# Kernel tuning notes

Measured on AMD Instinct MI355X. Metric: run time of the kernel, lower is better.

Reference implementation:

```python
import jax, jax.numpy as jnp
import numpy as np

N = 100000      # nodes
E = 1600000     # edges (avg degree 16)
F = 128         # nfeats
H = 4           # nheads
D = 16          # nhid // nheads
ALPHA = 0.2     # LeakyReLU negative slope


def setup_inputs() -> dict:
    key = jax.random.key(0)
    k0, k1, k2, k3, k4 = jax.random.split(key, 5)
    h = jax.random.normal(k0, (N, F), dtype=jnp.float32)
    src = jax.random.randint(k1, (E,), 0, N)
    dst = jax.random.randint(k2, (E,), 0, N)
    # per-head Linear W (xavier_uniform gain=1.414 approx) and attention vector a
    limW = 1.414 * np.sqrt(6.0 / (F + D))
    W = jax.random.uniform(k3, (H, F, D), jnp.float32, -limW, limW)
    Wb = jnp.zeros((H, D), jnp.float32)
    lima = 1.414 * np.sqrt(6.0 / (2 * D + 1))
    a = jax.random.uniform(k4, (H, 2 * D), jnp.float32, -lima, lima)
    ab = jnp.zeros((H,), jnp.float32)
    return {"h": h, "W": W, "Wb": Wb, "a": a, "ab": ab, "src": src, "dst": dst}


def reference(h, W, Wb, a, ab, src, dst):
    # Per-head linear projection (dropout is identity in eval mode)
    Wh = jnp.einsum('nf,hfd->nhd', h, W) + Wb          # [N,H,D]
    Whs = Wh[src]                                       # [E,H,D] gather src
    Whd = Wh[dst]                                       # [E,H,D] gather dst
    # e = leakyrelu(a . [Wh_src || Wh_dst])
    e = (jnp.einsum('ehd,hd->eh', Whs, a[:, :D]) +
         jnp.einsum('ehd,hd->eh', Whd, a[:, D:]) + ab)  # [E,H]
    e = jnp.where(e > 0, e, ALPHA * e)
    # segment softmax over incoming edges per dst node
    m = jax.ops.segment_max(e, dst, num_segments=N)     # [N,H]
    m = jnp.where(jnp.isfinite(m), m, 0.0)
    p = jnp.exp(e - m[dst])                             # [E,H]
    denom = jax.ops.segment_sum(p, dst, num_segments=N) # [N,H]
    num = jax.ops.segment_sum(p[:, :, None] * Whs, dst, num_segments=N)  # [N,H,D]
    h_prime = num / jnp.maximum(denom, 1e-9)[:, :, None]
    # concat heads -> [N, H*D]; rows of nodes with no in-edges are zero
    return h_prime.reshape(N, H * D)
```

## Files before the change

kernel.cpp:

```cpp
#include <hip/hip_runtime.h>
#include <hip/hip_bf16.h>
#include <math.h>

#define N_NODES 100000
#define N_EDGES 1600000
#define NF 128
#define NH 4
#define ND 16
#define GAT_ALPHA 0.2f

#define BSHIFT 8
#define NBK 391
#define CAPB 5120
#define CAPQ 1280
#define EPB 8192
#define EBLK 196
#define PBLK 391
#define NTILES ((N_NODES + 63) / 64)

typedef __attribute__((ext_vector_type(8))) __bf16 bf16x8;
typedef __attribute__((ext_vector_type(4))) float f32x4;

#define PADK 136

__global__ __launch_bounds__(256) void k_prep(
    const float* __restrict__ W, const float* __restrict__ a,
    int* __restrict__ gcur, __hip_bfloat16* __restrict__ Btg)
{
    const int hh = blockIdx.x;
    const int t = threadIdx.x;

    if (hh == 0)
        for (int i = t; i < 512; i += 256) gcur[i] = 0;

    for (int idx = t; idx < 2048; idx += 256) {
        int d = idx & 15, f = idx >> 4;
        Btg[(hh * 16 + d) * 128 + f] =
            __float2bfloat16(W[hh * (NF * ND) + f * ND + d]);
    }
    for (int idx = t; idx < 256; idx += 256) {
        int f = idx & 127, which = idx >> 7;
        float s = 0.f;
        #pragma unroll
        for (int d = 0; d < 16; d++)
            s = fmaf(W[hh * (NF * ND) + f * ND + d], a[hh * 32 + which * 16 + d], s);
        Btg[(64 + which * 8 + hh) * 128 + f] = __float2bfloat16(s);
    }
    for (int idx = t; idx < 256; idx += 256) {
        int f = idx & 127, which = idx >> 7;
        Btg[(68 + which * 8 + hh) * 128 + f] = __float2bfloat16(0.f);
    }
}

__global__ __launch_bounds__(256) void k_fused(
    const float* __restrict__ h, const __hip_bfloat16* __restrict__ Btg,
    const float* __restrict__ Wb, const float* __restrict__ a,
    const float* __restrict__ ab, const int* __restrict__ src,
    const int* __restrict__ dst, int* __restrict__ gcur,
    uint* __restrict__ sb, __hip_bfloat16* __restrict__ Whb,
    float* __restrict__ es, float* __restrict__ ed)
{
    __shared__ __align__(16) char smem[80 * PADK * 2];

    const int tid = threadIdx.x;

    if (blockIdx.x < EBLK) {
        int* hist = (int*)smem;
        int* cur  = hist + NBK;
        const int base = blockIdx.x * EPB;
        const int lim = min(EPB, N_EDGES - base);

        for (int i = tid; i < NBK; i += 256) hist[i] = 0;
        __syncthreads();
        for (int i = tid; i < lim; i += 256)
            atomicAdd(&hist[dst[base + i] >> BSHIFT], 1);
        __syncthreads();
        for (int i = tid; i < NBK; i += 256) {
            int v = hist[i];
            cur[i] = v ? atomicAdd(&gcur[i], v) : 0;
        }
        __syncthreads();
        for (int i = tid; i < lim; i += 256) {
            int d = dst[base + i];
            int bk = d >> BSHIFT;
            int pos = atomicAdd(&cur[bk], 1);
            if (pos < CAPB)
                sb[bk * CAPB + pos] = (uint)(src[base + i] | ((d & 255) << 17));
        }
        return;
    }

    __hip_bfloat16* Bt = (__hip_bfloat16*)smem;
    const int pb = blockIdx.x - EBLK;
    const int wv = tid >> 6;
    const int l = tid & 63;
    const int m = l & 15;
    const int quad = l >> 4;

    for (int c = tid; c < 80 * 128 / 8; c += 256) {
        int row = c >> 4, col = (c & 15) * 8;
        *(float4*)&Bt[row * PADK + col] = ((const float4*)Btg)[c];
    }

    float wb4[4];
    #pragma unroll
    for (int t = 0; t < 4; t++) wb4[t] = Wb[t * 16 + m];
    float eb = 0.f;
    if (m < 4) {
        #pragma unroll
        for (int d = 0; d < 16; d++) eb = fmaf(Wb[m * 16 + d], a[m * 32 + d], eb);
    } else if (m >= 8 && m < 12) {
        int hh = m - 8;
        #pragma unroll
        for (int d = 0; d < 16; d++)
            eb = fmaf(Wb[hh * 16 + d], a[hh * 32 + 16 + d], eb);
        eb += ab[hh];
    }
    __syncthreads();

    for (int tile = pb; tile < NTILES; tile += PBLK) {
        const int node = tile * 64 + wv * 16 + m;
        const bool ok = node < N_NODES;
        const float4* hrow = (const float4*)(h + (size_t)(ok ? node : 0) * NF);

        f32x4 acc[5];
        #pragma unroll
        for (int t = 0; t < 5; t++) acc[t] = (f32x4){0.f, 0.f, 0.f, 0.f};

        #pragma unroll
        for (int kk = 0; kk < 4; kk++) {
            bf16x8 af;
            if (ok) {
                float4 v0 = hrow[kk * 8 + quad * 2];
                float4 v1 = hrow[kk * 8 + quad * 2 + 1];
                af[0] = (__bf16)v0.x; af[1] = (__bf16)v0.y;
                af[2] = (__bf16)v0.z; af[3] = (__bf16)v0.w;
                af[4] = (__bf16)v1.x; af[5] = (__bf16)v1.y;
                af[6] = (__bf16)v1.z; af[7] = (__bf16)v1.w;
            } else {
                #pragma unroll
                for (int j = 0; j < 8; j++) af[j] = (__bf16)0.f;
            }
            #pragma unroll
            for (int t = 0; t < 5; t++) {
                bf16x8 bf = *(const bf16x8*)&Bt[(t * 16 + m) * PADK + kk * 32 + quad * 8];
                acc[t] = __builtin_amdgcn_mfma_f32_16x16x32_bf16(af, bf, acc[t], 0, 0, 0);
            }
        }

        const int nodeb = tile * 64 + wv * 16 + quad * 4;
        #pragma unroll
        for (int r = 0; r < 4; r++) {
            int n = nodeb + r;
            if (n < N_NODES) {
                #pragma unroll
                for (int t = 0; t < 4; t++)
                    Whb[n * 64 + t * 16 + m] = __float2bfloat16(acc[t][r] + wb4[t]);
                float ev = acc[4][r] + eb;
                if (m < 4) es[n * 4 + m] = ev;
                else if (m >= 8 && m < 12) ed[n * 4 + (m - 8)] = ev;
            }
        }
    }
}

__global__ __launch_bounds__(256) void k_bucket(
    const uint* __restrict__ sb, const int* __restrict__ gcur,
    const __hip_bfloat16* __restrict__ Whb, const float* __restrict__ es,
    const float* __restrict__ ed, float* __restrict__ out)
{
    __shared__ int ssl[CAPQ];
    __shared__ int ncnt[64];
    __shared__ int noff[64];
    __shared__ int ncur[64];
    __shared__ float pu_all[4][256];

    const int b  = blockIdx.x >> 2;
    const int qt = blockIdx.x & 3;
    const int t  = threadIdx.x;
    const int l  = t & 63;
    const int wid = t >> 6;

    const int ebase = b * CAPB;
    const int ecnt = min(gcur[b], CAPB);
    const int dlo = qt << 6;

    if (t < 64) ncnt[t] = 0;
    __syncthreads();

    for (int i = t; i < ecnt; i += 256) {
        int dn = (int)(sb[ebase + i] >> 17) - dlo;
        if ((unsigned)dn < 64u) atomicAdd(&ncnt[dn], 1);
    }
    __syncthreads();

    if (t < 64) {
        int v = ncnt[t];
        int x = v;
        #pragma unroll
        for (int o = 1; o < 64; o <<= 1) {
            int y = __shfl_up(x, o);
            if (l >= o) x += y;
        }
        noff[t] = x - v;
        ncur[t] = x - v;
    }
    __syncthreads();

    for (int i = t; i < ecnt; i += 256) {
        uint v = sb[ebase + i];
        int dn = (int)(v >> 17) - dlo;
        if ((unsigned)dn < 64u) {
            int pos = atomicAdd(&ncur[dn], 1);
            if (pos < CAPQ) ssl[pos] = (int)(v & 0x1FFFFu);
        }
    }
    __syncthreads();

    const int r = l & 15;
    const int q = l >> 4;
    const int hh = r >> 2;
    const float4* es4 = (const float4*)es;
    const uint2* Wu2 = (const uint2*)Whb;
    float* pu = &pu_all[wid][0];
    const float* pu_q = pu + q * 4 + hh;

    for (int k = 0; k < 16; k++) {
        const int ln = wid * 16 + k;
        const int node = b * 256 + dlo + ln;
        if (node >= N_NODES) break;

        int start = noff[ln];
        int deg = ncnt[ln];
        if (start >= CAPQ) deg = 0;
        else deg = min(deg, CAPQ - start);

        const float4 edv = ((const float4*)ed)[node];

        float acc0 = 0.f, acc1 = 0.f, acc2 = 0.f, acc3 = 0.f, den = 0.f;

        for (int bst = 0; bst < deg; bst += 64) {
            int nchunk = min(64, deg - bst);

            float4 p4 = make_float4(0.f, 0.f, 0.f, 0.f);
            if (l < nchunk) {
                int sl = ssl[start + bst + l];
                float4 esv = es4[sl];
                float x;
                x = esv.x + edv.x; p4.x = __expf(fmaxf(x, GAT_ALPHA * x));
                x = esv.y + edv.y; p4.y = __expf(fmaxf(x, GAT_ALPHA * x));
                x = esv.z + edv.z; p4.z = __expf(fmaxf(x, GAT_ALPHA * x));
                x = esv.w + edv.w; p4.w = __expf(fmaxf(x, GAT_ALPHA * x));
            }
            ((float4*)pu)[l] = p4;

            const int last = start + deg - 1;
            #pragma unroll 4
            for (int jj = 0; jj < nchunk; jj += 4) {
                int ee = min(start + bst + jj + q, last);
                int s = ssl[ee];
                float p = pu_q[jj * 4];
                uint2 v = Wu2[s * 16 + r];
                acc0 = fmaf(p, __uint_as_float(v.x << 16), acc0);
                acc1 = fmaf(p, __uint_as_float(v.x & 0xffff0000u), acc1);
                acc2 = fmaf(p, __uint_as_float(v.y << 16), acc2);
                acc3 = fmaf(p, __uint_as_float(v.y & 0xffff0000u), acc3);
                den += p;
            }
        }

        acc0 += __shfl_xor(acc0, 16); acc1 += __shfl_xor(acc1, 16);
        acc2 += __shfl_xor(acc2, 16); acc3 += __shfl_xor(acc3, 16);
        den  += __shfl_xor(den, 16);
        acc0 += __shfl_xor(acc0, 32); acc1 += __shfl_xor(acc1, 32);
        acc2 += __shfl_xor(acc2, 32); acc3 += __shfl_xor(acc3, 32);
        den  += __shfl_xor(den, 32);

        if (q == 0) {
            float rr = 1.0f / fmaxf(den, 1e-9f);
            ((float4*)out)[node * 16 + r] =
                make_float4(acc0 * rr, acc1 * rr, acc2 * rr, acc3 * rr);
        }
    }
}

extern "C" void kernel_launch(void* const* d_in, const int* in_sizes, int n_in,
                              void* d_out, int out_size, void* d_ws, size_t ws_size,
                              hipStream_t stream)
{
    const float* h  = (const float*)d_in[0];
    const float* W  = (const float*)d_in[1];
    const float* Wb = (const float*)d_in[2];
    const float* a  = (const float*)d_in[3];
    const float* ab = (const float*)d_in[4];
    const int* src  = (const int*)d_in[5];
    const int* dst  = (const int*)d_in[6];
    float* out = (float*)d_out;

    char* w = (char*)d_ws;
    __hip_bfloat16* Whb = (__hip_bfloat16*)w; w += (size_t)N_NODES * 64 * 2;
    float* es      = (float*)w;  w += (size_t)N_NODES * 4 * 4;
    float* ed      = (float*)w;  w += (size_t)N_NODES * 4 * 4;
    uint* sb       = (uint*)w;   w += (size_t)NBK * CAPB * 4;
    int* gcur      = (int*)w;    w += 512 * 4;
    __hip_bfloat16* Btg = (__hip_bfloat16*)w; w += 80 * 128 * 2;

    k_prep<<<4, 256, 0, stream>>>(W, a, gcur, Btg);
    k_fused<<<EBLK + PBLK, 256, 0, stream>>>(h, Btg, Wb, a, ab, src, dst,
                                             gcur, sb, Whb, es, ed);
    k_bucket<<<NBK * 4, 256, 0, stream>>>(sb, gcur, Whb, es, ed, out);
}
```

Before: 192.9 us.

## Give each projection tile its own block and widen gather to 16-byte loads

The projection part now launches one block per 64-node tile instead of a grid-stride loop, and issues the h row loads before the shared-memory weight staging so the global load latency overlaps that copy. The aggregation loop now has each lane gather 8 bf16 values (uint4) per source row instead of 4, covering 8 edges per wave step instead of 4. The shuffle reduction grows to three rounds over 9 values. This trades more blocks, each redoing the weight staging, and higher per-lane register use for fewer, wider memory transactions.

```diff
diff --git a/kernel.cpp b/kernel.cpp
--- a/kernel.cpp
+++ b/kernel.cpp
@@ -15,7 +15,7 @@
 #define CAPQ 1280
 #define EPB 8192
 #define EBLK 196
-#define PBLK 391
+#define PBLK 1563
 #define NTILES ((N_NODES + 63) / 64)
 
 typedef __attribute__((ext_vector_type(8))) __bf16 bf16x8;
@@ -91,12 +91,22 @@
     }
 
     __hip_bfloat16* Bt = (__hip_bfloat16*)smem;
-    const int pb = blockIdx.x - EBLK;
+    const int tile = blockIdx.x - EBLK;
     const int wv = tid >> 6;
     const int l = tid & 63;
     const int m = l & 15;
     const int quad = l >> 4;
 
+    const int node = tile * 64 + wv * 16 + m;
+    const bool ok = node < N_NODES;
+    const float4* hrow = (const float4*)(h + (size_t)(ok ? node : 0) * NF);
+    float4 va[8];
+    #pragma unroll
+    for (int kk = 0; kk < 4; kk++) {
+        va[kk * 2]     = hrow[kk * 8 + quad * 2];
+        va[kk * 2 + 1] = hrow[kk * 8 + quad * 2 + 1];
+    }
+
     for (int c = tid; c < 80 * 128 / 8; c += 256) {
         int row = c >> 4, col = (c & 15) * 8;
         *(float4*)&Bt[row * PADK + col] = ((const float4*)Btg)[c];
@@ -118,48 +128,41 @@
     }
     __syncthreads();
 
-    for (int tile = pb; tile < NTILES; tile += PBLK) {
-        const int node = tile * 64 + wv * 16 + m;
-        const bool ok = node < N_NODES;
-        const float4* hrow = (const float4*)(h + (size_t)(ok ? node : 0) * NF);
-
-        f32x4 acc[5];
-        #pragma unroll
-        for (int t = 0; t < 5; t++) acc[t] = (f32x4){0.f, 0.f, 0.f, 0.f};
-
-        #pragma unroll
-        for (int kk = 0; kk < 4; kk++) {
-            bf16x8 af;
-            if (ok) {
-                float4 v0 = hrow[kk * 8 + quad * 2];
-                float4 v1 = hrow[kk * 8 + quad * 2 + 1];
-                af[0] = (__bf16)v0.x; af[1] = (__bf16)v0.y;
-                af[2] = (__bf16)v0.z; af[3] = (__bf16)v0.w;
-                af[4] = (__bf16)v1.x; af[5] = (__bf16)v1.y;
-                af[6] = (__bf16)v1.z; af[7] = (__bf16)v1.w;
-            } else {
-                #pragma unroll
-                for (int j = 0; j < 8; j++) af[j] = (__bf16)0.f;
-            }
+    f32x4 acc[5];
+    #pragma unroll
+    for (int t = 0; t < 5; t++) acc[t] = (f32x4){0.f, 0.f, 0.f, 0.f};
+
+    #pragma unroll
+    for (int kk = 0; kk < 4; kk++) {
+        bf16x8 af;
+        if (ok) {
+            float4 v0 = va[kk * 2], v1 = va[kk * 2 + 1];
+            af[0] = (__bf16)v0.x; af[1] = (__bf16)v0.y;
+            af[2] = (__bf16)v0.z; af[3] = (__bf16)v0.w;
+            af[4] = (__bf16)v1.x; af[5] = (__bf16)v1.y;
+            af[6] = (__bf16)v1.z; af[7] = (__bf16)v1.w;
+        } else {
             #pragma unroll
-            for (int t = 0; t < 5; t++) {
-                bf16x8 bf = *(const bf16x8*)&Bt[(t * 16 + m) * PADK + kk * 32 + quad * 8];
-                acc[t] = __builtin_amdgcn_mfma_f32_16x16x32_bf16(af, bf, acc[t], 0, 0, 0);
-            }
-        }
-
-        const int nodeb = tile * 64 + wv * 16 + quad * 4;
-        #pragma unroll
-        for (int r = 0; r < 4; r++) {
-            int n = nodeb + r;
-            if (n < N_NODES) {
-                #pragma unroll
-                for (int t = 0; t < 4; t++)
-                    Whb[n * 64 + t * 16 + m] = __float2bfloat16(acc[t][r] + wb4[t]);
-                float ev = acc[4][r] + eb;
-                if (m < 4) es[n * 4 + m] = ev;
-                else if (m >= 8 && m < 12) ed[n * 4 + (m - 8)] = ev;
-            }
+            for (int j = 0; j < 8; j++) af[j] = (__bf16)0.f;
+        }
+        #pragma unroll
+        for (int t = 0; t < 5; t++) {
+            bf16x8 bf = *(const bf16x8*)&Bt[(t * 16 + m) * PADK + kk * 32 + quad * 8];
+            acc[t] = __builtin_amdgcn_mfma_f32_16x16x32_bf16(af, bf, acc[t], 0, 0, 0);
+        }
+    }
+
+    const int nodeb = tile * 64 + wv * 16 + quad * 4;
+    #pragma unroll
+    for (int r = 0; r < 4; r++) {
+        int n = nodeb + r;
+        if (n < N_NODES) {
+            #pragma unroll
+            for (int t = 0; t < 4; t++)
+                Whb[n * 64 + t * 16 + m] = __float2bfloat16(acc[t][r] + wb4[t]);
+            float ev = acc[4][r] + eb;
+            if (m < 4) es[n * 4 + m] = ev;
+            else if (m >= 8 && m < 12) ed[n * 4 + (m - 8)] = ev;
         }
     }
 }
@@ -217,13 +220,13 @@
     }
     __syncthreads();
 
-    const int r = l & 15;
-    const int q = l >> 4;
-    const int hh = r >> 2;
+    const int r8 = l & 7;
+    const int q8 = l >> 3;
+    const int hh8 = r8 >> 1;
     const float4* es4 = (const float4*)es;
-    const uint2* Wu2 = (const uint2*)Whb;
+    const uint4* Wu4 = (const uint4*)Whb;
     float* pu = &pu_all[wid][0];
-    const float* pu_q = pu + q * 4 + hh;
+    const float* pu_q8 = pu + q8 * 4 + hh8;
 
     for (int k = 0; k < 16; k++) {
         const int ln = wid * 16 + k;
@@ -237,7 +240,8 @@
 
         const float4 edv = ((const float4*)ed)[node];
 
-        float acc0 = 0.f, acc1 = 0.f, acc2 = 0.f, acc3 = 0.f, den = 0.f;
+        float ac0 = 0.f, ac1 = 0.f, ac2 = 0.f, ac3 = 0.f;
+        float ac4 = 0.f, ac5 = 0.f, ac6 = 0.f, ac7 = 0.f, den = 0.f;
 
         for (int bst = 0; bst < deg; bst += 64) {
             int nchunk = min(64, deg - bst);
@@ -256,30 +260,38 @@
 
             const int last = start + deg - 1;
             #pragma unroll 4
-            for (int jj = 0; jj < nchunk; jj += 4) {
-                int ee = min(start + bst + jj + q, last);
+            for (int jj = 0; jj < nchunk; jj += 8) {
+                int ee = min(start + bst + jj + q8, last);
                 int s = ssl[ee];
-                float p = pu_q[jj * 4];
-                uint2 v = Wu2[s * 16 + r];
-                acc0 = fmaf(p, __uint_as_float(v.x << 16), acc0);
-                acc1 = fmaf(p, __uint_as_float(v.x & 0xffff0000u), acc1);
-                acc2 = fmaf(p, __uint_as_float(v.y << 16), acc2);
-                acc3 = fmaf(p, __uint_as_float(v.y & 0xffff0000u), acc3);
+                float p = pu_q8[jj * 4];
+                uint4 v = Wu4[s * 8 + r8];
+                ac0 = fmaf(p, __uint_as_float(v.x << 16), ac0);
+                ac1 = fmaf(p, __uint_as_float(v.x & 0xffff0000u), ac1);
+                ac2 = fmaf(p, __uint_as_float(v.y << 16), ac2);
+                ac3 = fmaf(p, __uint_as_float(v.y & 0xffff0000u), ac3);
+                ac4 = fmaf(p, __uint_as_float(v.z << 16), ac4);
+                ac5 = fmaf(p, __uint_as_float(v.z & 0xffff0000u), ac5);
+                ac6 = fmaf(p, __uint_as_float(v.w << 16), ac6);
+                ac7 = fmaf(p, __uint_as_float(v.w & 0xffff0000u), ac7);
                 den += p;
             }
         }
 
-        acc0 += __shfl_xor(acc0, 16); acc1 += __shfl_xor(acc1, 16);
-        acc2 += __shfl_xor(acc2, 16); acc3 += __shfl_xor(acc3, 16);
-        den  += __shfl_xor(den, 16);
-        acc0 += __shfl_xor(acc0, 32); acc1 += __shfl_xor(acc1, 32);
-        acc2 += __shfl_xor(acc2, 32); acc3 += __shfl_xor(acc3, 32);
-        den  += __shfl_xor(den, 32);
-
-        if (q == 0) {
+        #pragma unroll
+        for (int o = 8; o < 64; o <<= 1) {
+            ac0 += __shfl_xor(ac0, o); ac1 += __shfl_xor(ac1, o);
+            ac2 += __shfl_xor(ac2, o); ac3 += __shfl_xor(ac3, o);
+            ac4 += __shfl_xor(ac4, o); ac5 += __shfl_xor(ac5, o);
+            ac6 += __shfl_xor(ac6, o); ac7 += __shfl_xor(ac7, o);
+            den += __shfl_xor(den, o);
+        }
+
+        if (q8 == 0) {
             float rr = 1.0f / fmaxf(den, 1e-9f);
-            ((float4*)out)[node * 16 + r] =
-                make_float4(acc0 * rr, acc1 * rr, acc2 * rr, acc3 * rr);
+            ((float4*)out)[node * 16 + r8 * 2] =
+                make_float4(ac0 * rr, ac1 * rr, ac2 * rr, ac3 * rr);
+            ((float4*)out)[node * 16 + r8 * 2 + 1] =
+                make_float4(ac4 * rr, ac5 * rr, ac6 * rr, ac7 * rr);
         }
     }
 }
```

Result: slower. 208.3 us (+8.0%).

## Process four destination nodes per wave with one quarter-wave per node

Applied to the files above, without the earlier changes.

The aggregation loop now gives each 16-lane quarter of a wave its own destination node, so a wave handles four nodes at once. Before, the whole wave worked on one node and needed cross-quarter shuffle reductions. The attention weights for all edges of the four nodes are computed together in one pass into a larger LDS buffer, which keeps more lanes busy than the old per-node 64-edge chunks. Destination scores are also preloaded into LDS once per block. The cost is serial per-lane loops whose length follows the largest degree in each group of four, and edges beyond 256 per group are silently dropped.

```diff
diff --git a/kernel.cpp b/kernel.cpp
--- a/kernel.cpp
+++ b/kernel.cpp
@@ -173,7 +173,8 @@
     __shared__ int ncnt[64];
     __shared__ int noff[64];
     __shared__ int ncur[64];
-    __shared__ float pu_all[4][256];
+    __shared__ float edl[64 * 4];
+    __shared__ float pu_all[4][256 * 4];
 
     const int b  = blockIdx.x >> 2;
     const int qt = blockIdx.x & 3;
@@ -185,7 +186,12 @@
     const int ecnt = min(gcur[b], CAPB);
     const int dlo = qt << 6;
 
-    if (t < 64) ncnt[t] = 0;
+    if (t < 64) {
+        ncnt[t] = 0;
+        int node = b * 256 + dlo + t;
+        ((float4*)edl)[t] = (node < N_NODES) ? ((const float4*)ed)[node]
+                                             : make_float4(0.f, 0.f, 0.f, 0.f);
+    }
     __syncthreads();
 
     for (int i = t; i < ecnt; i += 256) {
@@ -223,63 +229,63 @@
     const float4* es4 = (const float4*)es;
     const uint2* Wu2 = (const uint2*)Whb;
     float* pu = &pu_all[wid][0];
-    const float* pu_q = pu + q * 4 + hh;
-
-    for (int k = 0; k < 16; k++) {
-        const int ln = wid * 16 + k;
+
+    for (int kp = 0; kp < 4; kp++) {
+        const int base = wid * 16 + kp * 4;
+
+        int estart = min(noff[base], CAPQ);
+        int eend = min(noff[base + 3] + ncnt[base + 3], CAPQ);
+        int ecount = eend - estart;
+        if (ecount < 0) ecount = 0;
+        if (ecount > 256) ecount = 256;
+
+        const int off1 = noff[base + 1], off2 = noff[base + 2], off3 = noff[base + 3];
+
+        for (int e = l; e < ecount; e += 64) {
+            int gi = estart + e;
+            int sl = ssl[gi];
+            int nid = (gi >= off1) + (gi >= off2) + (gi >= off3);
+            const float4 edv = *(const float4*)&edl[(base + nid) * 4];
+            float4 esv = es4[sl];
+            float4 p4;
+            float x;
+            x = esv.x + edv.x; p4.x = __expf(fmaxf(x, GAT_ALPHA * x));
+            x = esv.y + edv.y; p4.y = __expf(fmaxf(x, GAT_ALPHA * x));
+            x = esv.z + edv.z; p4.z = __expf(fmaxf(x, GAT_ALPHA * x));
+            x = esv.w + edv.w; p4.w = __expf(fmaxf(x, GAT_ALPHA * x));
+            *(float4*)&pu[e * 4] = p4;
+        }
+
+        const int ln = base + q;
+        const int sbase = noff[ln];
+        int myoff = sbase - estart;
+        int deg = ncnt[ln];
+        if (sbase >= CAPQ) deg = 0;
+        else deg = min(deg, CAPQ - sbase);
+        {
+            int pucap = ecount - myoff;
+            if (pucap < 0) pucap = 0;
+            deg = min(deg, pucap);
+        }
+
+        float a0 = 0.f, a1 = 0.f, a2 = 0.f, a3 = 0.f, den = 0.f;
+        #pragma unroll 4
+        for (int j = 0; j < deg; j++) {
+            int s = ssl[sbase + j];
+            float p = pu[(myoff + j) * 4 + hh];
+            uint2 v = Wu2[s * 16 + r];
+            a0 = fmaf(p, __uint_as_float(v.x << 16), a0);
+            a1 = fmaf(p, __uint_as_float(v.x & 0xffff0000u), a1);
+            a2 = fmaf(p, __uint_as_float(v.y << 16), a2);
+            a3 = fmaf(p, __uint_as_float(v.y & 0xffff0000u), a3);
+            den += p;
+        }
+
         const int node = b * 256 + dlo + ln;
-        if (node >= N_NODES) break;
-
-        int start = noff[ln];
-        int deg = ncnt[ln];
-        if (start >= CAPQ) deg = 0;
-        else deg = min(deg, CAPQ - start);
-
-        const float4 edv = ((const float4*)ed)[node];
-
-        float acc0 = 0.f, acc1 = 0.f, acc2 = 0.f, acc3 = 0.f, den = 0.f;
-
-        for (int bst = 0; bst < deg; bst += 64) {
-            int nchunk = min(64, deg - bst);
-
-            float4 p4 = make_float4(0.f, 0.f, 0.f, 0.f);
-            if (l < nchunk) {
-                int sl = ssl[start + bst + l];
-                float4 esv = es4[sl];
-                float x;
-                x = esv.x + edv.x; p4.x = __expf(fmaxf(x, GAT_ALPHA * x));
-                x = esv.y + edv.y; p4.y = __expf(fmaxf(x, GAT_ALPHA * x));
-                x = esv.z + edv.z; p4.z = __expf(fmaxf(x, GAT_ALPHA * x));
-                x = esv.w + edv.w; p4.w = __expf(fmaxf(x, GAT_ALPHA * x));
-            }
-            ((float4*)pu)[l] = p4;
-
-            const int last = start + deg - 1;
-            #pragma unroll 4
-            for (int jj = 0; jj < nchunk; jj += 4) {
-                int ee = min(start + bst + jj + q, last);
-                int s = ssl[ee];
-                float p = pu_q[jj * 4];
-                uint2 v = Wu2[s * 16 + r];
-                acc0 = fmaf(p, __uint_as_float(v.x << 16), acc0);
-                acc1 = fmaf(p, __uint_as_float(v.x & 0xffff0000u), acc1);
-                acc2 = fmaf(p, __uint_as_float(v.y << 16), acc2);
-                acc3 = fmaf(p, __uint_as_float(v.y & 0xffff0000u), acc3);
-                den += p;
-            }
-        }
-
-        acc0 += __shfl_xor(acc0, 16); acc1 += __shfl_xor(acc1, 16);
-        acc2 += __shfl_xor(acc2, 16); acc3 += __shfl_xor(acc3, 16);
-        den  += __shfl_xor(den, 16);
-        acc0 += __shfl_xor(acc0, 32); acc1 += __shfl_xor(acc1, 32);
-        acc2 += __shfl_xor(acc2, 32); acc3 += __shfl_xor(acc3, 32);
-        den  += __shfl_xor(den, 32);
-
-        if (q == 0) {
+        if (node < N_NODES) {
             float rr = 1.0f / fmaxf(den, 1e-9f);
             ((float4*)out)[node * 16 + r] =
-                make_float4(acc0 * rr, acc1 * rr, acc2 * rr, acc3 * rr);
+                make_float4(a0 * rr, a1 * rr, a2 * rr, a3 * rr);
         }
     }
 }
```

Result: slower. 212.3 us (+10.0%).

## Fuse three kernels into one cooperative launch with grid-wide syncs

Applied to the files above, without the earlier changes.

Merges the prep, bucketing/projection, and per-bucket aggregation kernels into one cooperative kernel separated by grid.sync barriers, with a fallback to the original three launches. The aim is to remove two kernel launch gaps and the associated tail drain. In exchange, all 1564 blocks must be co-resident, so launch bounds force higher occupancy, which may cap registers. Grid barriers and idle blocks during the smaller phases add their own cost.

```diff
diff --git a/kernel.cpp b/kernel.cpp
--- a/kernel.cpp
+++ b/kernel.cpp
@@ -1,6 +1,9 @@
 #include <hip/hip_runtime.h>
 #include <hip/hip_bf16.h>
+#include <hip/hip_cooperative_groups.h>
 #include <math.h>
+
+namespace cg = cooperative_groups;
 
 #define N_NODES 100000
 #define N_EDGES 1600000
@@ -17,11 +20,270 @@
 #define EBLK 196
 #define PBLK 391
 #define NTILES ((N_NODES + 63) / 64)
+#define GRID_ALL (NBK * 4)
 
 typedef __attribute__((ext_vector_type(8))) __bf16 bf16x8;
 typedef __attribute__((ext_vector_type(4))) float f32x4;
 
 #define PADK 136
+
+__global__ __launch_bounds__(256, 8) void k_all(
+    const float* __restrict__ h, const float* __restrict__ W,
+    const float* __restrict__ Wb, const float* __restrict__ a,
+    const float* __restrict__ ab, const int* __restrict__ src,
+    const int* __restrict__ dst, int* __restrict__ gcur,
+    uint* __restrict__ sb, __hip_bfloat16* __restrict__ Whb,
+    float* __restrict__ es, float* __restrict__ ed,
+    __hip_bfloat16* __restrict__ Btg, float* __restrict__ out)
+{
+    cg::grid_group grid = cg::this_grid();
+    __shared__ __align__(16) char smem[80 * PADK * 2];
+
+    const int tid = threadIdx.x;
+    const int bid = blockIdx.x;
+    const int l = tid & 63;
+    const int wid = tid >> 6;
+
+    if (bid < 4) {
+        const int hh = bid;
+        if (hh == 0)
+            for (int i = tid; i < 512; i += 256) gcur[i] = 0;
+        for (int idx = tid; idx < 2048; idx += 256) {
+            int d = idx & 15, f = idx >> 4;
+            Btg[(hh * 16 + d) * 128 + f] =
+                __float2bfloat16(W[hh * (NF * ND) + f * ND + d]);
+        }
+        for (int idx = tid; idx < 256; idx += 256) {
+            int f = idx & 127, which = idx >> 7;
+            float s = 0.f;
+            #pragma unroll
+            for (int d = 0; d < 16; d++)
+                s = fmaf(W[hh * (NF * ND) + f * ND + d],
+                         a[hh * 32 + which * 16 + d], s);
+            Btg[(64 + which * 8 + hh) * 128 + f] = __float2bfloat16(s);
+        }
+        for (int idx = tid; idx < 256; idx += 256) {
+            int f = idx & 127, which = idx >> 7;
+            Btg[(68 + which * 8 + hh) * 128 + f] = __float2bfloat16(0.f);
+        }
+    }
+    grid.sync();
+
+    if (bid < EBLK) {
+        int* hist = (int*)smem;
+        int* cur  = hist + NBK;
+        const int base = bid * EPB;
+        const int lim = min(EPB, N_EDGES - base);
+
+        for (int i = tid; i < NBK; i += 256) hist[i] = 0;
+        __syncthreads();
+        for (int i = tid; i < lim; i += 256)
+            atomicAdd(&hist[dst[base + i] >> BSHIFT], 1);
+        __syncthreads();
+        for (int i = tid; i < NBK; i += 256) {
+            int v = hist[i];
+            cur[i] = v ? atomicAdd(&gcur[i], v) : 0;
+        }
+        __syncthreads();
+        for (int i = tid; i < lim; i += 256) {
+            int d = dst[base + i];
+            int bk = d >> BSHIFT;
+            int pos = atomicAdd(&cur[bk], 1);
+            if (pos < CAPB)
+                sb[bk * CAPB + pos] = (uint)(src[base + i] | ((d & 255) << 17));
+        }
+    } else if (bid < EBLK + PBLK) {
+        __hip_bfloat16* Bt = (__hip_bfloat16*)smem;
+        const int pb = bid - EBLK;
+        const int m = l & 15;
+        const int quad = l >> 4;
+
+        for (int c = tid; c < 80 * 128 / 8; c += 256) {
+            int row = c >> 4, col = (c & 15) * 8;
+            *(float4*)&Bt[row * PADK + col] = ((const float4*)Btg)[c];
+        }
+
+        float wb4[4];
+        #pragma unroll
+        for (int t = 0; t < 4; t++) wb4[t] = Wb[t * 16 + m];
+        float eb = 0.f;
+        if (m < 4) {
+            #pragma unroll
+            for (int d = 0; d < 16; d++)
+                eb = fmaf(Wb[m * 16 + d], a[m * 32 + d], eb);
+        } else if (m >= 8 && m < 12) {
+            int hh = m - 8;
+            #pragma unroll
+            for (int d = 0; d < 16; d++)
+                eb = fmaf(Wb[hh * 16 + d], a[hh * 32 + 16 + d], eb);
+            eb += ab[hh];
+        }
+        __syncthreads();
+
+        for (int tile = pb; tile < NTILES; tile += PBLK) {
+            const int node = tile * 64 + wid * 16 + m;
+            const bool ok = node < N_NODES;
+            const float4* hrow =
+                (const float4*)(h + (size_t)(ok ? node : 0) * NF);
+
+            f32x4 acc[5];
+            #pragma unroll
+            for (int t = 0; t < 5; t++) acc[t] = (f32x4){0.f, 0.f, 0.f, 0.f};
+
+            #pragma unroll
+            for (int kk = 0; kk < 4; kk++) {
+                bf16x8 af;
+                if (ok) {
+                    float4 v0 = hrow[kk * 8 + quad * 2];
+                    float4 v1 = hrow[kk * 8 + quad * 2 + 1];
+                    af[0] = (__bf16)v0.x; af[1] = (__bf16)v0.y;
+                    af[2] = (__bf16)v0.z; af[3] = (__bf16)v0.w;
+                    af[4] = (__bf16)v1.x; af[5] = (__bf16)v1.y;
+                    af[6] = (__bf16)v1.z; af[7] = (__bf16)v1.w;
+                } else {
+                    #pragma unroll
+                    for (int j = 0; j < 8; j++) af[j] = (__bf16)0.f;
+                }
+                #pragma unroll
+                for (int t = 0; t < 5; t++) {
+                    bf16x8 bf = *(const bf16x8*)
+                        &Bt[(t * 16 + m) * PADK + kk * 32 + quad * 8];
+                    acc[t] = __builtin_amdgcn_mfma_f32_16x16x32_bf16(
+                        af, bf, acc[t], 0, 0, 0);
+                }
+            }
+
+            const int nodeb = tile * 64 + wid * 16 + quad * 4;
+            #pragma unroll
+            for (int r = 0; r < 4; r++) {
+                int n = nodeb + r;
+                if (n < N_NODES) {
+                    #pragma unroll
+                    for (int t = 0; t < 4; t++)
+                        Whb[n * 64 + t * 16 + m] =
+                            __float2bfloat16(acc[t][r] + wb4[t]);
+                    float ev = acc[4][r] + eb;
+                    if (m < 4) es[n * 4 + m] = ev;
+                    else if (m >= 8 && m < 12) ed[n * 4 + (m - 8)] = ev;
+                }
+            }
+        }
+    }
+    grid.sync();
+
+    {
+        int* ssl  = (int*)smem;
+        int* ncnt = ssl + CAPQ;
+        int* noff = ncnt + 64;
+        int* ncur = noff + 64;
+        float* pu_all = (float*)(ncur + 64);
+
+        const int b  = bid >> 2;
+        const int qt = bid & 3;
+
+        const int ebase = b * CAPB;
+        const int ecnt = min(gcur[b], CAPB);
+        const int dlo = qt << 6;
+
+        if (tid < 64) ncnt[tid] = 0;
+        __syncthreads();
+
+        for (int i = tid; i < ecnt; i += 256) {
+            int dn = (int)(sb[ebase + i] >> 17) - dlo;
+            if ((unsigned)dn < 64u) atomicAdd(&ncnt[dn], 1);
+        }
+        __syncthreads();
+
+        if (tid < 64) {
+            int v = ncnt[tid];
+            int x = v;
+            #pragma unroll
+            for (int o = 1; o < 64; o <<= 1) {
+                int y = __shfl_up(x, o);
+                if (l >= o) x += y;
+            }
+            noff[tid] = x - v;
+            ncur[tid] = x - v;
+        }
+        __syncthreads();
+
+        for (int i = tid; i < ecnt; i += 256) {
+            uint v = sb[ebase + i];
+            int dn = (int)(v >> 17) - dlo;
+            if ((unsigned)dn < 64u) {
+                int pos = atomicAdd(&ncur[dn], 1);
+                if (pos < CAPQ) ssl[pos] = (int)(v & 0x1FFFFu);
+            }
+        }
+        __syncthreads();
+
+        const int r = l & 15;
+        const int q = l >> 4;
+        const int hh = r >> 2;
+        const float4* es4 = (const float4*)es;
+        const uint2* Wu2 = (const uint2*)Whb;
+        float* pu = pu_all + wid * 256;
+        const float* pu_q = pu + q * 4 + hh;
+
+        for (int k = 0; k < 16; k++) {
+            const int ln = wid * 16 + k;
+            const int node = b * 256 + dlo + ln;
+            if (node >= N_NODES) break;
+
+            int start = noff[ln];
+            int deg = ncnt[ln];
+            if (start >= CAPQ) deg = 0;
+            else deg = min(deg, CAPQ - start);
+
+            const float4 edv = ((const float4*)ed)[node];
+
+            float acc0 = 0.f, acc1 = 0.f, acc2 = 0.f, acc3 = 0.f, den = 0.f;
+
+            for (int bst = 0; bst < deg; bst += 64) {
+                int nchunk = min(64, deg - bst);
+
+                float4 p4 = make_float4(0.f, 0.f, 0.f, 0.f);
+                if (l < nchunk) {
+                    int sl = ssl[start + bst + l];
+                    float4 esv = es4[sl];
+                    float x;
+                    x = esv.x + edv.x; p4.x = __expf(fmaxf(x, GAT_ALPHA * x));
+                    x = esv.y + edv.y; p4.y = __expf(fmaxf(x, GAT_ALPHA * x));
+                    x = esv.z + edv.z; p4.z = __expf(fmaxf(x, GAT_ALPHA * x));
+                    x = esv.w + edv.w; p4.w = __expf(fmaxf(x, GAT_ALPHA * x));
+                }
+                ((float4*)pu)[l] = p4;
+
+                const int last = start + deg - 1;
+                #pragma unroll 4
+                for (int jj = 0; jj < nchunk; jj += 4) {
+                    int ee = min(start + bst + jj + q, last);
+                    int s = ssl[ee];
+                    float p = pu_q[jj * 4];
+                    uint2 v = Wu2[s * 16 + r];
+                    acc0 = fmaf(p, __uint_as_float(v.x << 16), acc0);
+                    acc1 = fmaf(p, __uint_as_float(v.x & 0xffff0000u), acc1);
+                    acc2 = fmaf(p, __uint_as_float(v.y << 16), acc2);
+                    acc3 = fmaf(p, __uint_as_float(v.y & 0xffff0000u), acc3);
+                    den += p;
+                }
+            }
+
+            acc0 += __shfl_xor(acc0, 16); acc1 += __shfl_xor(acc1, 16);
+            acc2 += __shfl_xor(acc2, 16); acc3 += __shfl_xor(acc3, 16);
+            den  += __shfl_xor(den, 16);
+            acc0 += __shfl_xor(acc0, 32); acc1 += __shfl_xor(acc1, 32);
+            acc2 += __shfl_xor(acc2, 32); acc3 += __shfl_xor(acc3, 32);
+            den  += __shfl_xor(den, 32);
+
+            if (q == 0) {
+                float rr = 1.0f / fmaxf(den, 1e-9f);
+                ((float4*)out)[node * 16 + r] =
+                    make_float4(acc0 * rr, acc1 * rr, acc2 * rr, acc3 * rr);
+            }
+        }
+    }
+}
 
 __global__ __launch_bounds__(256) void k_prep(
     const float* __restrict__ W, const float* __restrict__ a,
@@ -305,6 +567,26 @@
     int* gcur      = (int*)w;    w += 512 * 4;
     __hip_bfloat16* Btg = (__hip_bfloat16*)w; w += 80 * 128 * 2;
 
+    static int use_coop = -1;
+    if (use_coop < 0) {
+        int nb = 0;
+        hipError_t e = hipOccupancyMaxActiveBlocksPerMultiprocessor(
+            &nb, k_all, 256, 0);
+        use_coop = (e == hipSuccess && (long)nb * 256 >= GRID_ALL) ? 1 : 0;
+    }
+
+    if (use_coop) {
+        void* args[] = {
+            (void*)&h, (void*)&W, (void*)&Wb, (void*)&a, (void*)&ab,
+            (void*)&src, (void*)&dst, (void*)&gcur, (void*)&sb,
+            (void*)&Whb, (void*)&es, (void*)&ed, (void*)&Btg, (void*)&out};
+        hipError_t le = hipLaunchCooperativeKernel(
+            reinterpret_cast<void*>(k_all), dim3(GRID_ALL), dim3(256),
+            args, 0, stream);
+        if (le == hipSuccess) return;
+        use_coop = 0;
+    }
+
     k_prep<<<4, 256, 0, stream>>>(W, a, gcur, Btg);
     k_fused<<<EBLK + PBLK, 256, 0, stream>>>(h, Btg, Wb, a, ab, src, dst,
                                              gcur, sb, Whb, es, ed);
```

Result: slower. 199.5 us (+3.4%).
